# Kernel tuning notes

Hardware: AMD Instinct MI355X
Metric: run time of the kernel (lower is better)

Reference implementation:

```python
import jax, jax.numpy as jnp
import numpy as np

LN_EPS = 1e-5

def _layernorm(x, g, b):
    mu = jnp.mean(x, axis=-1, keepdims=True)
    var = jnp.mean(jnp.square(x - mu), axis=-1, keepdims=True)
    return (x - mu) * jax.lax.rsqrt(var + LN_EPS) * g + b


def setup_inputs() -> dict:
    key = jax.random.key(0)
    ks = jax.random.split(key, 8)
    B, N, F = 2, 100000, 128
    E, G = 400000, 10
    EMB, C = 32, 128
    features = jax.random.normal(ks[0], (B, N, F), dtype=jnp.float32)
    edge_index = jax.random.randint(ks[1], (2, E), 0, N, dtype=jnp.int32)
    lengths = jnp.full((G,), N // G, dtype=jnp.int32)
    emb_table = jax.random.normal(ks[2], (128, EMB), dtype=jnp.float32)
    W_in = jax.random.normal(ks[3], (F - 1 + EMB, C), dtype=jnp.float32) * (1.0 / np.sqrt(F - 1 + EMB))
    b_in = jnp.zeros((C,), jnp.float32)
    g_in = jnp.ones((C,), jnp.float32)
    beta_in = jnp.zeros((C,), jnp.float32)
    msg_W = jax.random.normal(ks[4], (3, C, C), dtype=jnp.float32) * (1.0 / np.sqrt(C))
    msg_b = jnp.zeros((3, C), jnp.float32)
    msg_g = jnp.ones((3, C), jnp.float32)
    msg_beta = jnp.zeros((3, C), jnp.float32)
    W_proj = jax.random.normal(ks[5], (C, 1), dtype=jnp.float32) * (1.0 / np.sqrt(C))
    b_proj = jnp.zeros((1,), jnp.float32)
    return {"features": features, "edge_index": edge_index, "lengths": lengths,
            "emb_table": emb_table, "W_in": W_in, "b_in": b_in, "g_in": g_in, "beta_in": beta_in,
            "msg_W": msg_W, "msg_b": msg_b, "msg_g": msg_g, "msg_beta": msg_beta,
            "W_proj": W_proj, "b_proj": b_proj}


def reference(features, edge_index, lengths, emb_table, W_in, b_in, g_in, beta_in,
              msg_W, msg_b, msg_g, msg_beta, W_proj, b_proj):
    B, N, F = features.shape
    rows, cols = edge_index[0], edge_index[1]

    # row-normalized sparse adjacency values (no grad path in original: torch.no_grad)
    ones = jnp.ones(rows.shape[0], dtype=features.dtype)
    deg = jax.ops.segment_sum(ones, rows, num_segments=N)
    vals = 1.0 / jnp.clip(deg, 1.0)[rows]  # [E]
    vals = jax.lax.stop_gradient(vals)

    # embedding input layer
    op = jnp.clip(features[..., 0].astype(jnp.int32), 0, emb_table.shape[0] - 1)  # [B,N]
    x = jnp.concatenate([emb_table[op], features[..., 1:]], axis=-1)  # [B,N,F-1+emb]
    x = _layernorm(jax.nn.silu(x @ W_in + b_in), g_in, beta_in)  # [B,N,C]

    # sparse message passing: agg[i] = sum_j A[i,j] x[j]
    for l in range(msg_W.shape[0]):
        msg = x[:, cols, :] * vals[None, :, None]  # [B,E,C]
        agg = jnp.zeros_like(x).at[:, rows, :].add(msg)  # scatter-sum to rows
        x = _layernorm(jax.nn.silu(agg @ msg_W[l] + msg_b[l]), msg_g[l], msg_beta[l])

    # ragged graph pooling over node axis
    G = lengths.shape[0]
    index = jnp.asarray(np.repeat(np.arange(G), np.asarray(lengths)))  # [N]
    pooled = jax.ops.segment_sum(x.transpose(1, 0, 2), index, num_segments=G)  # [G,B,C]
    runtimes = pooled @ W_proj + b_proj  # [G,B,1]
    return runtimes[..., 0]  # [G,B]
```

## Files before the change

### kernel.cpp

```cpp
#include <hip/hip_runtime.h>
#include <cstddef>

#define LN_EPS 1e-5f
typedef unsigned short u16;
typedef unsigned int u32;
typedef __attribute__((ext_vector_type(8))) short bf16x8;
typedef __attribute__((ext_vector_type(4))) float f32x4;

constexpr int SCAN_T = 256, SCAN_V = 8, SCAN_ELEMS = SCAN_T * SCAN_V;
constexpr int KP = 136;

__device__ inline u16 f2bf(float f) {
    u32 u = __float_as_uint(f);
    u += 0x7FFFu + ((u >> 16) & 1u);
    return (u16)(u >> 16);
}
__device__ inline float bf2f(u16 h) { return __uint_as_float((u32)h << 16); }

__device__ inline void acc_u4(float* a, uint4 u) {
    a[0] += bf2f((u16)(u.x & 0xFFFF)); a[1] += bf2f((u16)(u.x >> 16));
    a[2] += bf2f((u16)(u.y & 0xFFFF)); a[3] += bf2f((u16)(u.y >> 16));
    a[4] += bf2f((u16)(u.z & 0xFFFF)); a[5] += bf2f((u16)(u.z >> 16));
    a[6] += bf2f((u16)(u.w & 0xFFFF)); a[7] += bf2f((u16)(u.w >> 16));
}

__global__ __launch_bounds__(256) void k_deg(const int* __restrict__ rows,
                                             int* __restrict__ deg, int E) {
    int e = blockIdx.x * 256 + threadIdx.x;
    if (e < E) atomicAdd(&deg[rows[e]], 1);
}

__global__ __launch_bounds__(256) void k_invdeg(const int* __restrict__ deg,
                                                float* __restrict__ invdeg, int N) {
    int i = blockIdx.x * 256 + threadIdx.x;
    if (i < N) invdeg[i] = 1.0f / (float)max(deg[i], 1);
}

__global__ __launch_bounds__(SCAN_T) void k_scan1(const int* __restrict__ deg,
                                                  int* __restrict__ row_ptr,
                                                  int* __restrict__ bsum, int N) {
    __shared__ int ts[SCAN_T];
    int t = threadIdx.x;
    int base = blockIdx.x * SCAN_ELEMS;
    int v[SCAN_V];
    int s = 0;
    #pragma unroll
    for (int j = 0; j < SCAN_V; ++j) {
        int i = base + t * SCAN_V + j;
        v[j] = (i < N) ? deg[i] : 0;
        s += v[j];
    }
    ts[t] = s;
    __syncthreads();
    for (int off = 1; off < SCAN_T; off <<= 1) {
        int val = (t >= off) ? ts[t - off] : 0;
        __syncthreads();
        ts[t] += val;
        __syncthreads();
    }
    int excl = (t > 0) ? ts[t - 1] : 0;
    #pragma unroll
    for (int j = 0; j < SCAN_V; ++j) {
        int i = base + t * SCAN_V + j;
        if (i < N) row_ptr[i] = excl;
        excl += v[j];
    }
    if (t == SCAN_T - 1) bsum[blockIdx.x] = ts[SCAN_T - 1];
}

__global__ void k_scan2(int* __restrict__ bsum, int nb, int* __restrict__ row_ptr, int N) {
    int run = 0;
    for (int i = 0; i < nb; ++i) {
        int v = bsum[i];
        bsum[i] = run;
        run += v;
    }
    row_ptr[N] = run;
}

__global__ __launch_bounds__(SCAN_T) void k_scan3(int* __restrict__ row_ptr,
                                                  const int* __restrict__ bsum, int N) {
    int add = bsum[blockIdx.x];
    int base = blockIdx.x * SCAN_ELEMS;
    #pragma unroll
    for (int j = 0; j < SCAN_V; ++j) {
        int i = base + threadIdx.x * SCAN_V + j;
        if (i < N) row_ptr[i] += add;
    }
}

__global__ __launch_bounds__(256) void k_copy_cursor(const int* __restrict__ row_ptr,
                                                     int* __restrict__ cursor, int N) {
    int i = blockIdx.x * 256 + threadIdx.x;
    if (i < N) cursor[i] = row_ptr[i];
}

__global__ __launch_bounds__(256) void k_bucket(const int* __restrict__ rows,
                                                const int* __restrict__ cols,
                                                int* __restrict__ cursor,
                                                int* __restrict__ col_sorted, int E) {
    int e = blockIdx.x * 256 + threadIdx.x;
    if (e < E) {
        int r = rows[e];
        int pos = atomicAdd(&cursor[r], 1);
        col_sorted[pos] = cols[e];
    }
}

__global__ __launch_bounds__(256) void k_wprep(const float* __restrict__ W_in,
                                               const float* __restrict__ msg_W,
                                               u16* __restrict__ Wt_in,
                                               u16* __restrict__ Wt_msg) {
    int idx = blockIdx.x * 256 + threadIdx.x;
    const int t1 = 128 * 128;
    if (idx < t1) {
        int c = idx >> 7, k = idx & 127;
        float v = (k >= 1) ? W_in[(31 + k) * 128 + c] : 0.f;
        Wt_in[idx] = f2bf(v);
    } else {
        idx -= t1;
        if (idx < 3 * 128 * 128) {
            int l = idx / (128 * 128);
            int r = idx & (128 * 128 - 1);
            int c = r >> 7, k = r & 127;
            Wt_msg[idx] = f2bf(msg_W[l * 16384 + k * 128 + c]);
        }
    }
}

__global__ __launch_bounds__(128) void k_eproj(const float* __restrict__ W_in,
                                               const float* __restrict__ emb,
                                               float* __restrict__ E_proj) {
    __shared__ float es[32];
    int op = blockIdx.x, c = threadIdx.x;
    if (c < 32) es[c] = emb[op * 32 + c];
    __syncthreads();
    float s = 0.f;
    #pragma unroll
    for (int j = 0; j < 32; ++j) s = fmaf(es[j], W_in[j * 128 + c], s);
    E_proj[op * 128 + c] = s;
}

__global__ __launch_bounds__(256) void k_input_mfma(
    const float* __restrict__ features, const float* __restrict__ E_proj,
    const u16* __restrict__ Wt,
    const float* __restrict__ bias, const float* __restrict__ gain,
    const float* __restrict__ beta, u16* __restrict__ x, int N, int ntiles)
{
    __shared__ u16 A[64 * KP];
    __shared__ u16 Wl[128 * KP];
    __shared__ int ops[64];
    const int tid = threadIdx.x;
    const int lane = tid & 63, w = tid >> 6;
    const int l15 = lane & 15;
    const int kq = (lane >> 4) * 8;
    const int r = tid >> 2, q = tid & 3;

    for (int i = tid; i < 2048; i += 256) {
        uint4 v = ((const uint4*)Wt)[i];
        *(uint4*)&Wl[(i >> 4) * KP + (i & 15) * 8] = v;
    }
    float bsr[8], gsr[8], btr[8];
    #pragma unroll
    for (int t = 0; t < 8; ++t) {
        int col = t * 16 + l15;
        bsr[t] = bias[col]; gsr[t] = gain[col]; btr[t] = beta[col];
    }

    for (int tile = blockIdx.x; tile < ntiles; tile += gridDim.x) {
        const int node0 = tile * 32;
        __syncthreads();
        {
            int nl = r >> 1, b = r & 1;
            int node = min(node0 + nl, N - 1);
            const float* fr = features + ((size_t)b * N + node) * 128 + q * 32;
            u32 pk[16];
            float4 v0 = ((const float4*)fr)[0];
            if (q == 0) {
                int op = (int)v0.x;
                op = op < 0 ? 0 : (op > 127 ? 127 : op);
                ops[r] = op;
            }
            pk[0] = (u32)f2bf(v0.x) | ((u32)f2bf(v0.y) << 16);
            pk[1] = (u32)f2bf(v0.z) | ((u32)f2bf(v0.w) << 16);
            #pragma unroll
            for (int j = 1; j < 8; ++j) {
                float4 v = ((const float4*)fr)[j];
                pk[2 * j]     = (u32)f2bf(v.x) | ((u32)f2bf(v.y) << 16);
                pk[2 * j + 1] = (u32)f2bf(v.z) | ((u32)f2bf(v.w) << 16);
            }
            uint4* dst = (uint4*)&A[r * KP + q * 32];
            #pragma unroll
            for (int j = 0; j < 4; ++j)
                dst[j] = make_uint4(pk[4 * j], pk[4 * j + 1], pk[4 * j + 2], pk[4 * j + 3]);
        }
        __syncthreads();

        const int arow = w * 16 + l15;
        bf16x8 a[4];
        #pragma unroll
        for (int kt = 0; kt < 4; ++kt)
            a[kt] = *(const bf16x8*)&A[arow * KP + kt * 32 + kq];
        f32x4 acc[8];
        #pragma unroll
        for (int t = 0; t < 8; ++t) {
            f32x4 c4 = {0.f, 0.f, 0.f, 0.f};
            #pragma unroll
            for (int kt = 0; kt < 4; ++kt) {
                bf16x8 b = *(const bf16x8*)&Wl[(t * 16 + l15) * KP + kt * 32 + kq];
                c4 = __builtin_amdgcn_mfma_f32_16x16x32_bf16(a[kt], b, c4, 0, 0, 0);
            }
            acc[t] = c4;
        }

        int opr[4];
        #pragma unroll
        for (int i = 0; i < 4; ++i) opr[i] = ops[w * 16 + (lane >> 4) * 4 + i];

        float s[4] = {0, 0, 0, 0}, sq[4] = {0, 0, 0, 0};
        #pragma unroll
        for (int t = 0; t < 8; ++t) {
            int col = t * 16 + l15;
            #pragma unroll
            for (int i = 0; i < 4; ++i) {
                float aY = acc[t][i] + bsr[t] + E_proj[opr[i] * 128 + col];
                float y = aY / (1.0f + __expf(-aY));
                acc[t][i] = y;
                s[i] += y;
                sq[i] = fmaf(y, y, sq[i]);
            }
        }
        #pragma unroll
        for (int m = 1; m <= 8; m <<= 1) {
            #pragma unroll
            for (int i = 0; i < 4; ++i) {
                s[i] += __shfl_xor(s[i], m);
                sq[i] += __shfl_xor(sq[i], m);
            }
        }
        #pragma unroll
        for (int i = 0; i < 4; ++i) {
            float mu = s[i] * (1.0f / 128.0f);
            float var = sq[i] * (1.0f / 128.0f) - mu * mu;
            float inv = rsqrtf(var + LN_EPS);
            int rr = w * 16 + (lane >> 4) * 4 + i;
            if (node0 + (rr >> 1) < N) {
                u16* xr = x + ((size_t)node0 * 2 + rr) * 128;
                #pragma unroll
                for (int t = 0; t < 8; ++t)
                    xr[t * 16 + l15] = f2bf((acc[t][i] - mu) * inv * gsr[t] + btr[t]);
            }
        }
    }
}

__global__ __launch_bounds__(256) void k_mp_mfma(
    const int* __restrict__ row_ptr, const int* __restrict__ col_sorted,
    const float* __restrict__ invdeg, const u16* __restrict__ xin,
    const u16* __restrict__ Wt, const float* __restrict__ bias,
    const float* __restrict__ gain, const float* __restrict__ beta,
    u16* __restrict__ xout, int N, int ntiles)
{
    __shared__ u16 A[64 * KP];
    __shared__ u16 Wl[128 * KP];
    const int tid = threadIdx.x;
    const int lane = tid & 63, w = tid >> 6;
    const int l15 = lane & 15;
    const int kq = (lane >> 4) * 8;
    const int r = tid >> 2, q = tid & 3;

    for (int i = tid; i < 2048; i += 256) {
        uint4 v = ((const uint4*)Wt)[i];
        *(uint4*)&Wl[(i >> 4) * KP + (i & 15) * 8] = v;
    }

    for (int tile = blockIdx.x; tile < ntiles; tile += gridDim.x) {
        const int node0 = tile * 32;
        __syncthreads();
        {
            int nl = r >> 1, b = r & 1;
            int node = min(node0 + nl, N - 1);
            int e0 = row_ptr[node], e1 = row_ptr[node + 1];
            float sc = invdeg[node];
            const u32* xb = (const u32*)xin + (size_t)b * 64 + q * 16;
            float fa[32];
            #pragma unroll
            for (int j = 0; j < 32; ++j) fa[j] = 0.f;
            int e = e0;
            for (; e + 2 <= e1; e += 2) {
                int c0 = col_sorted[e], c1 = col_sorted[e + 1];
                const uint4* p0 = (const uint4*)(xb + (size_t)c0 * 128);
                const uint4* p1 = (const uint4*)(xb + (size_t)c1 * 128);
                uint4 u0 = p0[0], u1 = p0[1], u2 = p0[2], u3 = p0[3];
                uint4 w0 = p1[0], w1 = p1[1], w2 = p1[2], w3 = p1[3];
                acc_u4(fa + 0, u0);  acc_u4(fa + 8, u1);
                acc_u4(fa + 16, u2); acc_u4(fa + 24, u3);
                acc_u4(fa + 0, w0);  acc_u4(fa + 8, w1);
                acc_u4(fa + 16, w2); acc_u4(fa + 24, w3);
            }
            if (e < e1) {
                const uint4* p0 = (const uint4*)(xb + (size_t)col_sorted[e] * 128);
                uint4 u0 = p0[0], u1 = p0[1], u2 = p0[2], u3 = p0[3];
                acc_u4(fa + 0, u0);  acc_u4(fa + 8, u1);
                acc_u4(fa + 16, u2); acc_u4(fa + 24, u3);
            }
            u32 pk[16];
            #pragma unroll
            for (int j = 0; j < 16; ++j)
                pk[j] = (u32)f2bf(fa[2 * j] * sc) | ((u32)f2bf(fa[2 * j + 1] * sc) << 16);
            uint4* dst = (uint4*)&A[r * KP + q * 32];
            #pragma unroll
            for (int j = 0; j < 4; ++j)
                dst[j] = make_uint4(pk[4 * j], pk[4 * j + 1], pk[4 * j + 2], pk[4 * j + 3]);
        }
        __syncthreads();

        const int arow = w * 16 + l15;
        bf16x8 a[4];
        #pragma unroll
        for (int kt = 0; kt < 4; ++kt)
            a[kt] = *(const bf16x8*)&A[arow * KP + kt * 32 + kq];
        f32x4 acc[8];
        #pragma unroll
        for (int t = 0; t < 8; ++t) {
            f32x4 c4 = {0.f, 0.f, 0.f, 0.f};
            #pragma unroll
            for (int kt = 0; kt < 4; ++kt) {
                bf16x8 bfr = *(const bf16x8*)&Wl[(t * 16 + l15) * KP + kt * 32 + kq];
                c4 = __builtin_amdgcn_mfma_f32_16x16x32_bf16(a[kt], bfr, c4, 0, 0, 0);
            }
            acc[t] = c4;
        }

        float s[4] = {0, 0, 0, 0}, sq[4] = {0, 0, 0, 0};
        #pragma unroll
        for (int t = 0; t < 8; ++t) {
            int col = t * 16 + l15;
            float bt = bias[col];
            #pragma unroll
            for (int i = 0; i < 4; ++i) {
                float aY = acc[t][i] + bt;
                float y = aY / (1.0f + __expf(-aY));
                acc[t][i] = y;
                s[i] += y;
                sq[i] = fmaf(y, y, sq[i]);
            }
        }
        #pragma unroll
        for (int m = 1; m <= 8; m <<= 1) {
            #pragma unroll
            for (int i = 0; i < 4; ++i) {
                s[i] += __shfl_xor(s[i], m);
                sq[i] += __shfl_xor(sq[i], m);
            }
        }
        #pragma unroll
        for (int i = 0; i < 4; ++i) {
            float mu = s[i] * (1.0f / 128.0f);
            float var = sq[i] * (1.0f / 128.0f) - mu * mu;
            float inv = rsqrtf(var + LN_EPS);
            int rr = w * 16 + (lane >> 4) * 4 + i;
            if (node0 + (rr >> 1) < N) {
                u16* xr = xout + ((size_t)node0 * 2 + rr) * 128;
                #pragma unroll
                for (int t = 0; t < 8; ++t) {
                    int col = t * 16 + l15;
                    xr[col] = f2bf((acc[t][i] - mu) * inv * gain[col] + beta[col]);
                }
            }
        }
    }
}

__global__ __launch_bounds__(64) void k_pool(
    const u16* __restrict__ x, const int* __restrict__ lengths,
    float* __restrict__ pooled, int N, int B, int G, int SPLIT)
{
    int blk = blockIdx.x;
    int split = blk % SPLIT;
    int gb = blk / SPLIT;
    int b = gb % B, g = gb / B;
    int lane = threadIdx.x;
    int start = 0;
    for (int i = 0; i < g; ++i) start += lengths[i];
    int len = lengths[g];
    int chunk = (len + SPLIT - 1) / SPLIT;
    int n0 = start + split * chunk;
    int n1 = min(start + len, n0 + chunk);
    const u32* xb = (const u32*)x + (size_t)b * 64;
    float sx = 0.f, sy = 0.f;
    int n = n0;
    for (; n + 4 <= n1; n += 4) {
        u32 v0 = xb[(size_t)(n + 0) * 128 + lane];
        u32 v1 = xb[(size_t)(n + 1) * 128 + lane];
        u32 v2 = xb[(size_t)(n + 2) * 128 + lane];
        u32 v3 = xb[(size_t)(n + 3) * 128 + lane];
        sx += bf2f((u16)(v0 & 0xFFFF)) + bf2f((u16)(v1 & 0xFFFF)) +
              bf2f((u16)(v2 & 0xFFFF)) + bf2f((u16)(v3 & 0xFFFF));
        sy += bf2f((u16)(v0 >> 16)) + bf2f((u16)(v1 >> 16)) +
              bf2f((u16)(v2 >> 16)) + bf2f((u16)(v3 >> 16));
    }
    for (; n < n1; ++n) {
        u32 v = xb[(size_t)n * 128 + lane];
        sx += bf2f((u16)(v & 0xFFFF));
        sy += bf2f((u16)(v >> 16));
    }
    if (n1 > n0) {
        atomicAdd(&pooled[(g * B + b) * 128 + lane * 2 + 0], sx);
        atomicAdd(&pooled[(g * B + b) * 128 + lane * 2 + 1], sy);
    }
}

__global__ __launch_bounds__(128) void k_proj(
    const float* __restrict__ pooled, const float* __restrict__ Wp,
    const float* __restrict__ bp, float* __restrict__ out, int GB)
{
    int gb = blockIdx.x;
    int tid = threadIdx.x;
    float v = pooled[gb * 128 + tid] * Wp[tid];
    v += __shfl_down(v, 32);
    v += __shfl_down(v, 16);
    v += __shfl_down(v, 8);
    v += __shfl_down(v, 4);
    v += __shfl_down(v, 2);
    v += __shfl_down(v, 1);
    __shared__ float red[2];
    if ((tid & 63) == 0) red[tid >> 6] = v;
    __syncthreads();
    if (tid == 0) out[gb] = red[0] + red[1] + bp[0];
}

extern "C" void kernel_launch(void* const* d_in, const int* in_sizes, int n_in,
                              void* d_out, int out_size, void* d_ws, size_t ws_size,
                              hipStream_t stream) {
    const float* features = (const float*)d_in[0];
    const int* edge_index = (const int*)d_in[1];
    const int* lengths    = (const int*)d_in[2];
    const float* emb      = (const float*)d_in[3];
    const float* W_in     = (const float*)d_in[4];
    const float* b_in     = (const float*)d_in[5];
    const float* g_in     = (const float*)d_in[6];
    const float* beta_in  = (const float*)d_in[7];
    const float* msg_W    = (const float*)d_in[8];
    const float* msg_b    = (const float*)d_in[9];
    const float* msg_g    = (const float*)d_in[10];
    const float* msg_beta = (const float*)d_in[11];
    const float* W_proj   = (const float*)d_in[12];
    const float* b_proj   = (const float*)d_in[13];
    float* out = (float*)d_out;

    const int E = in_sizes[1] / 2;
    const int G = in_sizes[2];
    const int B = out_size / G;
    const int C = in_sizes[5];
    const int F = 128;
    const int N = in_sizes[0] / (B * F);
    const int M = B * N;
    const int L = in_sizes[9] / C;

    const int* rows = edge_index;
    const int* cols = edge_index + E;

    u16* buf0   = (u16*)d_ws;
    u16* buf1   = buf0 + (size_t)M * 128;
    u16* Wt_in  = buf1 + (size_t)M * 128;
    u16* Wt_msg = Wt_in + 128 * 128;
    float* E_proj = (float*)(Wt_msg + 3 * 128 * 128);
    float* invdeg = E_proj + 128 * 128;
    int*   deg    = (int*)(invdeg + N);
    float* pooled = (float*)(deg + N);
    int*   row_ptr = (int*)(pooled + (size_t)G * B * 128);
    int*   col_sorted = row_ptr + N + 1;
    int*   bsum   = col_sorted + E;

    const int nb_scan = (N + SCAN_ELEMS - 1) / SCAN_ELEMS;
    const int nt32 = (N + 31) / 32;
    const int grid_mp = nt32 < 1024 ? nt32 : 1024;

    {
        int total = 4 * 128 * 128;
        k_wprep<<<(total + 255) / 256, 256, 0, stream>>>(W_in, msg_W, Wt_in, Wt_msg);
        k_eproj<<<128, 128, 0, stream>>>(W_in, emb, E_proj);
    }

    hipMemsetAsync(deg, 0, (size_t)N * sizeof(int), stream);
    k_deg<<<(E + 255) / 256, 256, 0, stream>>>(rows, deg, E);
    k_invdeg<<<(N + 255) / 256, 256, 0, stream>>>(deg, invdeg, N);
    k_scan1<<<nb_scan, SCAN_T, 0, stream>>>(deg, row_ptr, bsum, N);
    k_scan2<<<1, 1, 0, stream>>>(bsum, nb_scan, row_ptr, N);
    k_scan3<<<nb_scan, SCAN_T, 0, stream>>>(row_ptr, bsum, N);
    k_copy_cursor<<<(N + 255) / 256, 256, 0, stream>>>(row_ptr, deg, N);
    k_bucket<<<(E + 255) / 256, 256, 0, stream>>>(rows, cols, deg, col_sorted, E);

    k_input_mfma<<<grid_mp, 256, 0, stream>>>(features, E_proj, Wt_in,
                                              b_in, g_in, beta_in, buf0, N, nt32);

    u16* bufs[2] = {buf0, buf1};
    int cur = 0;
    for (int l = 0; l < L; ++l) {
        k_mp_mfma<<<grid_mp, 256, 0, stream>>>(row_ptr, col_sorted, invdeg,
                                               bufs[cur], Wt_msg + (size_t)l * 128 * 128,
                                               msg_b + (size_t)l * C, msg_g + (size_t)l * C,
                                               msg_beta + (size_t)l * C,
                                               bufs[1 - cur], N, nt32);
        cur = 1 - cur;
    }

    const int SPLIT = 128;
    hipMemsetAsync(pooled, 0, (size_t)G * B * 128 * sizeof(float), stream);
    k_pool<<<G * B * SPLIT, 64, 0, stream>>>(bufs[cur], lengths, pooled, N, B, G, SPLIT);
    k_proj<<<G * B, 128, 0, stream>>>(pooled, W_proj, b_proj, out, G * B);
}
```

Baseline: 359.1 us.

## Widen message-passing blocks to 512 threads and split gather and MFMA columns

The message-passing kernel now launches 512 threads per block. Each gather thread handles 16 feature columns instead of 32, and the eight waves split the 128 output columns into two halves for the MFMA tile. Per-row LayerNorm partial sums are combined through a small shared-memory buffer with an extra barrier, which replaces the barrier at the top of the loop. The aim is more memory-level parallelism and lower register pressure in the latency-bound neighbor gather. The cost is an extra synchronization and a cross-wave reduction per tile.

```diff
diff --git a/kernel.cpp b/kernel.cpp
--- a/kernel.cpp
+++ b/kernel.cpp
@@ -254,7 +254,7 @@
     }
 }
 
-__global__ __launch_bounds__(256) void k_mp_mfma(
+__global__ __launch_bounds__(512, 6) void k_mp_mfma(
     const int* __restrict__ row_ptr, const int* __restrict__ col_sorted,
     const float* __restrict__ invdeg, const u16* __restrict__ xin,
     const u16* __restrict__ Wt, const float* __restrict__ bias,
@@ -263,70 +263,68 @@
 {
     __shared__ u16 A[64 * KP];
     __shared__ u16 Wl[128 * KP];
+    __shared__ float pS[64][2], pQ[64][2];
     const int tid = threadIdx.x;
     const int lane = tid & 63, w = tid >> 6;
     const int l15 = lane & 15;
     const int kq = (lane >> 4) * 8;
-    const int r = tid >> 2, q = tid & 3;
-
-    for (int i = tid; i < 2048; i += 256) {
+    const int r = tid >> 3, sl = tid & 7;
+    const int wr = w & 3, wc = w >> 2;
+
+    for (int i = tid; i < 2048; i += 512) {
         uint4 v = ((const uint4*)Wt)[i];
         *(uint4*)&Wl[(i >> 4) * KP + (i & 15) * 8] = v;
     }
 
     for (int tile = blockIdx.x; tile < ntiles; tile += gridDim.x) {
         const int node0 = tile * 32;
-        __syncthreads();
         {
             int nl = r >> 1, b = r & 1;
             int node = min(node0 + nl, N - 1);
             int e0 = row_ptr[node], e1 = row_ptr[node + 1];
             float sc = invdeg[node];
-            const u32* xb = (const u32*)xin + (size_t)b * 64 + q * 16;
-            float fa[32];
-            #pragma unroll
-            for (int j = 0; j < 32; ++j) fa[j] = 0.f;
+            const u32* xb = (const u32*)xin + (size_t)b * 64 + sl * 8;
+            float fa[16];
+            #pragma unroll
+            for (int j = 0; j < 16; ++j) fa[j] = 0.f;
             int e = e0;
             for (; e + 2 <= e1; e += 2) {
                 int c0 = col_sorted[e], c1 = col_sorted[e + 1];
                 const uint4* p0 = (const uint4*)(xb + (size_t)c0 * 128);
                 const uint4* p1 = (const uint4*)(xb + (size_t)c1 * 128);
-                uint4 u0 = p0[0], u1 = p0[1], u2 = p0[2], u3 = p0[3];
-                uint4 w0 = p1[0], w1 = p1[1], w2 = p1[2], w3 = p1[3];
-                acc_u4(fa + 0, u0);  acc_u4(fa + 8, u1);
-                acc_u4(fa + 16, u2); acc_u4(fa + 24, u3);
-                acc_u4(fa + 0, w0);  acc_u4(fa + 8, w1);
-                acc_u4(fa + 16, w2); acc_u4(fa + 24, w3);
+                uint4 u0 = p0[0], u1 = p0[1];
+                uint4 w0 = p1[0], w1 = p1[1];
+                acc_u4(fa, u0);     acc_u4(fa + 8, u1);
+                acc_u4(fa, w0);     acc_u4(fa + 8, w1);
             }
             if (e < e1) {
                 const uint4* p0 = (const uint4*)(xb + (size_t)col_sorted[e] * 128);
-                uint4 u0 = p0[0], u1 = p0[1], u2 = p0[2], u3 = p0[3];
-                acc_u4(fa + 0, u0);  acc_u4(fa + 8, u1);
-                acc_u4(fa + 16, u2); acc_u4(fa + 24, u3);
-            }
-            u32 pk[16];
-            #pragma unroll
-            for (int j = 0; j < 16; ++j)
+                uint4 u0 = p0[0], u1 = p0[1];
+                acc_u4(fa, u0);     acc_u4(fa + 8, u1);
+            }
+            u32 pk[8];
+            #pragma unroll
+            for (int j = 0; j < 8; ++j)
                 pk[j] = (u32)f2bf(fa[2 * j] * sc) | ((u32)f2bf(fa[2 * j + 1] * sc) << 16);
-            uint4* dst = (uint4*)&A[r * KP + q * 32];
-            #pragma unroll
-            for (int j = 0; j < 4; ++j)
-                dst[j] = make_uint4(pk[4 * j], pk[4 * j + 1], pk[4 * j + 2], pk[4 * j + 3]);
+            uint4* dst = (uint4*)&A[r * KP + sl * 16];
+            dst[0] = make_uint4(pk[0], pk[1], pk[2], pk[3]);
+            dst[1] = make_uint4(pk[4], pk[5], pk[6], pk[7]);
         }
         __syncthreads();
 
-        const int arow = w * 16 + l15;
+        const int arow = wr * 16 + l15;
         bf16x8 a[4];
         #pragma unroll
         for (int kt = 0; kt < 4; ++kt)
             a[kt] = *(const bf16x8*)&A[arow * KP + kt * 32 + kq];
-        f32x4 acc[8];
-        #pragma unroll
-        for (int t = 0; t < 8; ++t) {
+        f32x4 acc[4];
+        #pragma unroll
+        for (int t = 0; t < 4; ++t) {
+            int bcol = wc * 64 + t * 16 + l15;
             f32x4 c4 = {0.f, 0.f, 0.f, 0.f};
             #pragma unroll
             for (int kt = 0; kt < 4; ++kt) {
-                bf16x8 bfr = *(const bf16x8*)&Wl[(t * 16 + l15) * KP + kt * 32 + kq];
+                bf16x8 bfr = *(const bf16x8*)&Wl[bcol * KP + kt * 32 + kq];
                 c4 = __builtin_amdgcn_mfma_f32_16x16x32_bf16(a[kt], bfr, c4, 0, 0, 0);
             }
             acc[t] = c4;
@@ -334,8 +332,8 @@
 
         float s[4] = {0, 0, 0, 0}, sq[4] = {0, 0, 0, 0};
         #pragma unroll
-        for (int t = 0; t < 8; ++t) {
-            int col = t * 16 + l15;
+        for (int t = 0; t < 4; ++t) {
+            int col = wc * 64 + t * 16 + l15;
             float bt = bias[col];
             #pragma unroll
             for (int i = 0; i < 4; ++i) {
@@ -354,17 +352,29 @@
                 sq[i] += __shfl_xor(sq[i], m);
             }
         }
+        if (l15 == 0) {
+            #pragma unroll
+            for (int i = 0; i < 4; ++i) {
+                int rr = wr * 16 + (lane >> 4) * 4 + i;
+                pS[rr][wc] = s[i];
+                pQ[rr][wc] = sq[i];
+            }
+        }
+        __syncthreads();
+
         #pragma unroll
         for (int i = 0; i < 4; ++i) {
-            float mu = s[i] * (1.0f / 128.0f);
-            float var = sq[i] * (1.0f / 128.0f) - mu * mu;
+            int rr = wr * 16 + (lane >> 4) * 4 + i;
+            float st = pS[rr][0] + pS[rr][1];
+            float qt = pQ[rr][0] + pQ[rr][1];
+            float mu = st * (1.0f / 128.0f);
+            float var = qt * (1.0f / 128.0f) - mu * mu;
             float inv = rsqrtf(var + LN_EPS);
-            int rr = w * 16 + (lane >> 4) * 4 + i;
             if (node0 + (rr >> 1) < N) {
                 u16* xr = xout + ((size_t)node0 * 2 + rr) * 128;
                 #pragma unroll
-                for (int t = 0; t < 8; ++t) {
-                    int col = t * 16 + l15;
+                for (int t = 0; t < 4; ++t) {
+                    int col = wc * 64 + t * 16 + l15;
                     xr[col] = f2bf((acc[t][i] - mu) * inv * gain[col] + beta[col]);
                 }
             }
@@ -498,7 +508,7 @@
     u16* bufs[2] = {buf0, buf1};
     int cur = 0;
     for (int l = 0; l < L; ++l) {
-        k_mp_mfma<<<grid_mp, 256, 0, stream>>>(row_ptr, col_sorted, invdeg,
+        k_mp_mfma<<<grid_mp, 512, 0, stream>>>(row_ptr, col_sorted, invdeg,
                                                bufs[cur], Wt_msg + (size_t)l * 128 * 128,
                                                msg_b + (size_t)l * C, msg_g + (size_t)l * C,
                                                msg_beta + (size_t)l * C,
```

New measurement: 371.2 us. +3.4%, slower.
